# Optimization experiments

Measured on AMD Instinct MI355X. Metric: run time of the kernel, lower is better.

The kernel has to match this reference:

```python
import jax, jax.numpy as jnp
import numpy as np

B, H, S, O = 16384, 512, 6, 1


def setup_inputs() -> dict:
    key = jax.random.key(0)
    ks = jax.random.split(key, 14)
    w = lambda k, shape: jax.random.normal(k, shape, dtype=jnp.float32) * 0.02
    return {
        "input": jax.random.normal(ks[0], (B, O), dtype=jnp.float32),
        "hidden": jax.random.normal(ks[1], (B, H), dtype=jnp.float32),
        "cell": jax.random.normal(ks[2], (B, H), dtype=jnp.float32),
        "encoder_outputs": jax.random.normal(ks[3], (B, S, H), dtype=jnp.float32),
        # attn: Linear(2H+O -> S)
        "W_attn": w(ks[4], (S, 2 * H + O)),
        "b_attn": w(ks[5], (S,)),
        # attn_combine: Linear(H+O -> H)
        "W_comb": w(ks[6], (H, H + O)),
        "b_comb": w(ks[7], (H,)),
        # LSTM(H -> H), torch gate order i,f,g,o
        "W_ih": w(ks[8], (4 * H, H)),
        "W_hh": w(ks[9], (4 * H, H)),
        "b_ih": w(ks[10], (4 * H,)),
        "b_hh": w(ks[11], (4 * H,)),
        # out: Linear(H -> O)
        "W_out": w(ks[12], (O, H)),
        "b_out": w(ks[13], (O,)),
    }


def reference(input, hidden, cell, encoder_outputs,
              W_attn, b_attn, W_comb, b_comb,
              W_ih, W_hh, b_ih, b_hh, W_out, b_out):
    # Bahdanau-style attention over encoder outputs (eval mode: dropout = identity)
    attn_in = jnp.concatenate([input, hidden, cell], axis=1)          # [B, 2H+O]
    attn_weights = jax.nn.softmax(attn_in @ W_attn.T + b_attn, axis=1)  # [B, S]
    attn_applied = jnp.einsum("bs,bsh->bh", attn_weights, encoder_outputs)  # [B, H]

    x = jnp.concatenate([input, attn_applied], axis=1)                # [B, H+O]
    x = jax.nn.relu(x @ W_comb.T + b_comb)                            # [B, H]

    # single LSTM step (torch gate order: i, f, g, o)
    gates = x @ W_ih.T + b_ih + hidden @ W_hh.T + b_hh               # [B, 4H]
    i, f, g, o = jnp.split(gates, 4, axis=1)
    c_new = jax.nn.sigmoid(f) * cell + jax.nn.sigmoid(i) * jnp.tanh(g)
    h_new = jax.nn.sigmoid(o) * jnp.tanh(c_new)

    output = h_new @ W_out.T + b_out                                  # [B, O]
    return output, h_new, c_new, attn_weights[:, None, :]
```

## Files before the change

kernel.cpp:

```cpp
#include <hip/hip_runtime.h>
#include <hip/hip_bf16.h>

typedef __attribute__((ext_vector_type(8))) short frag8;
typedef __attribute__((ext_vector_type(4))) float f32x4;

#define ASYNC16(gsrc, ldst) \
  __builtin_amdgcn_global_load_lds((const __attribute__((address_space(1))) void*)(gsrc), \
                                   (__attribute__((address_space(3))) void*)(ldst), 16, 0, 0)

__device__ __forceinline__ float sigmoid_(float x) { return 1.0f / (1.0f + __expf(-x)); }
__device__ __forceinline__ float tanh_(float x)    { return 1.0f - 2.0f / (__expf(2.0f * x) + 1.0f); }

__global__ __launch_bounds__(256) void prep_kernel(
    const float* __restrict__ W_comb, const float* __restrict__ W_ih,
    const float* __restrict__ W_hh, const float* __restrict__ b_ih,
    const float* __restrict__ b_hh,
    __hip_bfloat16* __restrict__ Wc, __hip_bfloat16* __restrict__ Wg,
    float* __restrict__ biasg)
{
  int idx = blockIdx.x * 256 + threadIdx.x;
  const int NW = 2048 * 1024, NC = 512 * 512;
  if (idx < NW) {
    int np = idx >> 10, k = idx & 1023;
    int u = np >> 2, j = np & 3;
    int n = j * 512 + u;
    float v = (k < 512) ? W_ih[n * 512 + k] : W_hh[n * 512 + (k - 512)];
    Wg[idx] = __float2bfloat16(v);
  } else if (idx < NW + NC) {
    int t = idx - NW;
    int n = t >> 9, k = t & 511;
    Wc[t] = __float2bfloat16(W_comb[n * 513 + 1 + k]);
  } else if (idx < NW + NC + 2048) {
    int np = idx - NW - NC;
    int u = np >> 2, j = np & 3;
    int n = j * 512 + u;
    biasg[np] = b_ih[n] + b_hh[n];
  }
}

__global__ __launch_bounds__(256) void attn_kernel(
    const float* __restrict__ inputv, const float* __restrict__ hidden,
    const float* __restrict__ cell, const float* __restrict__ enc,
    const float* __restrict__ W_attn, const float* __restrict__ b_attn,
    __hip_bfloat16* __restrict__ A1, __hip_bfloat16* __restrict__ Z,
    float* __restrict__ outA)
{
  __shared__ float Wl[6 * 1025];
  const int tid = threadIdx.x;
  for (int i = tid; i < 6 * 1025; i += 256) Wl[i] = W_attn[i];
  __syncthreads();
  const int w = tid >> 6, lane = tid & 63;
  const long row = (long)blockIdx.x * 4 + w;

  const float* hp = hidden + row * 512;
  const float* cp = cell + row * 512;
  float h8[8];
  float acc[6] = {0.f, 0.f, 0.f, 0.f, 0.f, 0.f};
#pragma unroll
  for (int i = 0; i < 8; ++i) {
    int k = lane + i * 64;
    float hv = hp[k], cv = cp[k];
    h8[i] = hv;
#pragma unroll
    for (int s = 0; s < 6; ++s)
      acc[s] += hv * Wl[s * 1025 + 1 + k] + cv * Wl[s * 1025 + 513 + k];
  }
  float iv = inputv[row];
  float logit[6];
#pragma unroll
  for (int s = 0; s < 6; ++s) {
    float a = acc[s];
#pragma unroll
    for (int d = 32; d > 0; d >>= 1) a += __shfl_xor(a, d);
    logit[s] = a + iv * Wl[s * 1025] + b_attn[s];
  }
  float mx = logit[0];
#pragma unroll
  for (int s = 1; s < 6; ++s) mx = fmaxf(mx, logit[s]);
  float wts[6], tot = 0.f;
#pragma unroll
  for (int s = 0; s < 6; ++s) { wts[s] = __expf(logit[s] - mx); tot += wts[s]; }
  float rt = 1.f / tot;
#pragma unroll
  for (int s = 0; s < 6; ++s) wts[s] *= rt;
  if (lane < 6) {
    float mw = 0.f;
#pragma unroll
    for (int s = 0; s < 6; ++s) if (lane == s) mw = wts[s];
    outA[row * 6 + lane] = mw;
  }
  const float* ep = enc + row * 3072;
#pragma unroll
  for (int i = 0; i < 8; ++i) {
    int k = lane + i * 64;
    float a = 0.f;
#pragma unroll
    for (int s = 0; s < 6; ++s) a += wts[s] * ep[s * 512 + k];
    A1[row * 512 + k] = __float2bfloat16(a);
    Z[row * 1024 + 512 + k] = __float2bfloat16(h8[i]);
  }
}

__device__ __forceinline__ void stage16(const __hip_bfloat16* __restrict__ g, int ld,
                                        int row0, int k0, __hip_bfloat16* lds, int tid)
{
  int c0 = tid, c1 = tid + 256;
  const __hip_bfloat16* g0 = g + (long)(row0 + (c0 >> 2)) * ld + k0 + (c0 & 3) * 8;
  const __hip_bfloat16* g1 = g + (long)(row0 + (c1 >> 2)) * ld + k0 + (c1 & 3) * 8;
  char* l0 = (char*)lds + (tid & ~63) * 16;
  ASYNC16(g0, l0);
  ASYNC16(g1, l0 + 4096);
}

__global__ __launch_bounds__(256) void comb_gemm(
    const __hip_bfloat16* __restrict__ A, const __hip_bfloat16* __restrict__ Bt,
    const float* __restrict__ b_comb, const float* __restrict__ W_comb,
    const float* __restrict__ inputv, __hip_bfloat16* __restrict__ Z)
{
  __shared__ __align__(16) __hip_bfloat16 As[128 * 32];
  __shared__ __align__(16) __hip_bfloat16 Bs[128 * 32];
  const int tid = threadIdx.x;
  const int lane = tid & 63, w = tid >> 6;
  const int quad = lane >> 4, l15 = lane & 15;
  const int m0 = blockIdx.y * 128, n0 = blockIdx.x * 128;
  const int wm = (w & 1) * 64, wn = (w >> 1) * 64;

  f32x4 acc[4][4] = {};
  for (int kt = 0; kt < 16; ++kt) {
    int k0 = kt * 32;
    stage16(A, 512, m0, k0, As, tid);
    stage16(Bt, 512, n0, k0, Bs, tid);
    __syncthreads();
    frag8 af[4], bf[4];
#pragma unroll
    for (int i = 0; i < 4; ++i)
      af[i] = *(const frag8*)((const short*)As + (wm + i * 16 + l15) * 32 + quad * 8);
#pragma unroll
    for (int j = 0; j < 4; ++j)
      bf[j] = *(const frag8*)((const short*)Bs + (wn + j * 16 + l15) * 32 + quad * 8);
#pragma unroll
    for (int i = 0; i < 4; ++i)
#pragma unroll
      for (int j = 0; j < 4; ++j)
        acc[i][j] = __builtin_amdgcn_mfma_f32_16x16x32_bf16(af[i], bf[j], acc[i][j], 0, 0, 0);
    __syncthreads();
  }
  float bc[4], w0[4];
#pragma unroll
  for (int j = 0; j < 4; ++j) {
    int col = n0 + wn + j * 16 + l15;
    bc[j] = b_comb[col];
    w0[j] = W_comb[col * 513];
  }
#pragma unroll
  for (int i = 0; i < 4; ++i) {
#pragma unroll
    for (int r = 0; r < 4; ++r) {
      int row = m0 + wm + i * 16 + quad * 4 + r;
      float iv = inputv[row];
#pragma unroll
      for (int j = 0; j < 4; ++j) {
        int col = n0 + wn + j * 16 + l15;
        float v = acc[i][j][r] + bc[j] + iv * w0[j];
        Z[(long)row * 1024 + col] = __float2bfloat16(fmaxf(v, 0.0f));
      }
    }
  }
}

__global__ __launch_bounds__(256) void gates_gemm(
    const __hip_bfloat16* __restrict__ Zm, const __hip_bfloat16* __restrict__ Wg,
    const float* __restrict__ biasg, const float* __restrict__ cell,
    float* __restrict__ outH, float* __restrict__ outC)
{
  __shared__ __align__(16) float smemf[64 * 132];
  __hip_bfloat16* As = (__hip_bfloat16*)smemf;
  __hip_bfloat16* Bs = (__hip_bfloat16*)smemf + 4096;
  float* Cl = smemf;
  const int tid = threadIdx.x;
  const int lane = tid & 63, w = tid >> 6;
  const int quad = lane >> 4, l15 = lane & 15;
  const int m0 = blockIdx.y * 128, n0 = blockIdx.x * 128;
  const int wm = (w & 1) * 64, wn = (w >> 1) * 64;

  f32x4 acc[4][4] = {};
  for (int kt = 0; kt < 32; ++kt) {
    int k0 = kt * 32;
    stage16(Zm, 1024, m0, k0, As, tid);
    stage16(Wg, 1024, n0, k0, Bs, tid);
    __syncthreads();
    frag8 af[4], bf[4];
#pragma unroll
    for (int i = 0; i < 4; ++i)
      af[i] = *(const frag8*)((const short*)As + (wm + i * 16 + l15) * 32 + quad * 8);
#pragma unroll
    for (int j = 0; j < 4; ++j)
      bf[j] = *(const frag8*)((const short*)Bs + (wn + j * 16 + l15) * 32 + quad * 8);
#pragma unroll
    for (int i = 0; i < 4; ++i)
#pragma unroll
      for (int j = 0; j < 4; ++j)
        acc[i][j] = __builtin_amdgcn_mfma_f32_16x16x32_bf16(af[i], bf[j], acc[i][j], 0, 0, 0);
    __syncthreads();
  }
  for (int hh = 0; hh < 2; ++hh) {
    if ((w & 1) == hh) {
#pragma unroll
      for (int i = 0; i < 4; ++i)
#pragma unroll
        for (int j = 0; j < 4; ++j)
#pragma unroll
          for (int r = 0; r < 4; ++r)
            Cl[(i * 16 + quad * 4 + r) * 132 + wn + j * 16 + l15] = acc[i][j][r];
    }
    __syncthreads();
#pragma unroll
    for (int it = 0; it < 8; ++it) {
      int p = tid + it * 256;
      int rl = p >> 5, ul = p & 31;
      long row = m0 + hh * 64 + rl;
      int u = (n0 >> 2) + ul;
      float4 gv = *(const float4*)(Cl + rl * 132 + ul * 4);
      float4 bv = *(const float4*)(biasg + n0 + ul * 4);
      float ig = gv.x + bv.x, fg = gv.y + bv.y, gg = gv.z + bv.z, og = gv.w + bv.w;
      float cv = cell[row * 512 + u];
      float cn = sigmoid_(fg) * cv + sigmoid_(ig) * tanh_(gg);
      float hn = sigmoid_(og) * tanh_(cn);
      outH[row * 512 + u] = hn;
      outC[row * 512 + u] = cn;
    }
    __syncthreads();
  }
}

__global__ __launch_bounds__(256) void out_gemv(
    const float* __restrict__ h, const float* __restrict__ W_out,
    const float* __restrict__ b_out, float* __restrict__ out)
{
  __shared__ float wl[512];
  const int tid = threadIdx.x;
  for (int i = tid; i < 512; i += 256) wl[i] = W_out[i];
  __syncthreads();
  const int w = tid >> 6, lane = tid & 63;
  const long row = (long)blockIdx.x * 4 + w;
  float s = 0.f;
#pragma unroll
  for (int i = 0; i < 8; ++i) {
    int k = lane + i * 64;
    s += h[row * 512 + k] * wl[k];
  }
#pragma unroll
  for (int d = 32; d > 0; d >>= 1) s += __shfl_xor(s, d);
  if (lane == 0) out[row] = s + b_out[0];
}

extern "C" void kernel_launch(void* const* d_in, const int* in_sizes, int n_in,
                              void* d_out, int out_size, void* d_ws, size_t ws_size,
                              hipStream_t stream) {
  const float* inputv = (const float*)d_in[0];
  const float* hidden = (const float*)d_in[1];
  const float* cell   = (const float*)d_in[2];
  const float* enc    = (const float*)d_in[3];
  const float* W_attn = (const float*)d_in[4];
  const float* b_attn = (const float*)d_in[5];
  const float* W_comb = (const float*)d_in[6];
  const float* b_comb = (const float*)d_in[7];
  const float* W_ih   = (const float*)d_in[8];
  const float* W_hh   = (const float*)d_in[9];
  const float* b_ih   = (const float*)d_in[10];
  const float* b_hh   = (const float*)d_in[11];
  const float* W_out  = (const float*)d_in[12];
  const float* b_out  = (const float*)d_in[13];

  float* out  = (float*)d_out;
  float* outO = out;
  float* outH = out + 16384;
  float* outC = out + 8404992;
  float* outA = out + 16793600;

  char* ws = (char*)d_ws;
  __hip_bfloat16* Z   = (__hip_bfloat16*)ws;
  __hip_bfloat16* A1  = (__hip_bfloat16*)(ws + 33554432);
  __hip_bfloat16* Wc  = (__hip_bfloat16*)(ws + 50331648);
  __hip_bfloat16* Wg  = (__hip_bfloat16*)(ws + 50855936);
  float*          bg  = (float*)(ws + 55050240);

  prep_kernel<<<9224, 256, 0, stream>>>(W_comb, W_ih, W_hh, b_ih, b_hh, Wc, Wg, bg);
  attn_kernel<<<4096, 256, 0, stream>>>(inputv, hidden, cell, enc, W_attn, b_attn, A1, Z, outA);
  comb_gemm<<<dim3(4, 128), 256, 0, stream>>>(A1, Wc, b_comb, W_comb, inputv, Z);
  gates_gemm<<<dim3(16, 128), 256, 0, stream>>>(Z, Wg, bg, cell, outH, outC);
  out_gemv<<<4096, 256, 0, stream>>>(outH, W_out, b_out, outO);
}
```

Before: 532.7 us.

## Reorder gate weight interleave for direct epilogue, vectorize loads, widen GEMM K-step

```diff
diff --git a/kernel.cpp b/kernel.cpp
--- a/kernel.cpp
+++ b/kernel.cpp
@@ -22,7 +22,8 @@
   const int NW = 2048 * 1024, NC = 512 * 512;
   if (idx < NW) {
     int np = idx >> 10, k = idx & 1023;
-    int u = np >> 2, j = np & 3;
+    int j = (np >> 4) & 3;
+    int u = ((np >> 6) << 4) | (np & 15);
     int n = j * 512 + u;
     float v = (k < 512) ? W_ih[n * 512 + k] : W_hh[n * 512 + (k - 512)];
     Wg[idx] = __float2bfloat16(v);
@@ -32,7 +33,8 @@
     Wc[t] = __float2bfloat16(W_comb[n * 513 + 1 + k]);
   } else if (idx < NW + NC + 2048) {
     int np = idx - NW - NC;
-    int u = np >> 2, j = np & 3;
+    int j = (np >> 4) & 3;
+    int u = ((np >> 6) << 4) | (np & 15);
     int n = j * 512 + u;
     biasg[np] = b_ih[n] + b_hh[n];
   }
@@ -45,25 +47,34 @@
     __hip_bfloat16* __restrict__ A1, __hip_bfloat16* __restrict__ Z,
     float* __restrict__ outA)
 {
-  __shared__ float Wl[6 * 1025];
+  __shared__ float Wlh[6 * 1024];
+  __shared__ float Wl0[6];
   const int tid = threadIdx.x;
-  for (int i = tid; i < 6 * 1025; i += 256) Wl[i] = W_attn[i];
+  for (int i = tid; i < 6 * 1024; i += 256) {
+    int s = i >> 10, k = i & 1023;
+    Wlh[i] = W_attn[s * 1025 + 1 + k];
+  }
+  if (tid < 6) Wl0[tid] = W_attn[tid * 1025];
   __syncthreads();
   const int w = tid >> 6, lane = tid & 63;
   const long row = (long)blockIdx.x * 4 + w;
-
-  const float* hp = hidden + row * 512;
-  const float* cp = cell + row * 512;
-  float h8[8];
-  float acc[6] = {0.f, 0.f, 0.f, 0.f, 0.f, 0.f};
-#pragma unroll
-  for (int i = 0; i < 8; ++i) {
-    int k = lane + i * 64;
-    float hv = hp[k], cv = cp[k];
-    h8[i] = hv;
-#pragma unroll
-    for (int s = 0; s < 6; ++s)
-      acc[s] += hv * Wl[s * 1025 + 1 + k] + cv * Wl[s * 1025 + 513 + k];
+  const int k8 = lane * 8;
+
+  const float4* hp4 = (const float4*)(hidden + row * 512 + k8);
+  const float4* cp4 = (const float4*)(cell + row * 512 + k8);
+  float4 h0 = hp4[0], h1 = hp4[1];
+  float4 c0 = cp4[0], c1 = cp4[1];
+
+  float acc[6];
+#pragma unroll
+  for (int s = 0; s < 6; ++s) {
+    const float4* wh = (const float4*)(Wlh + s * 1024 + k8);
+    const float4* wc = (const float4*)(Wlh + s * 1024 + 512 + k8);
+    float4 a0 = wh[0], a1 = wh[1], b0 = wc[0], b1 = wc[1];
+    acc[s] = h0.x * a0.x + h0.y * a0.y + h0.z * a0.z + h0.w * a0.w
+           + h1.x * a1.x + h1.y * a1.y + h1.z * a1.z + h1.w * a1.w
+           + c0.x * b0.x + c0.y * b0.y + c0.z * b0.z + c0.w * b0.w
+           + c1.x * b1.x + c1.y * b1.y + c1.z * b1.z + c1.w * b1.w;
   }
   float iv = inputv[row];
   float logit[6];
@@ -72,7 +83,7 @@
     float a = acc[s];
 #pragma unroll
     for (int d = 32; d > 0; d >>= 1) a += __shfl_xor(a, d);
-    logit[s] = a + iv * Wl[s * 1025] + b_attn[s];
+    logit[s] = a + iv * Wl0[s] + b_attn[s];
   }
   float mx = logit[0];
 #pragma unroll
@@ -89,16 +100,22 @@
     for (int s = 0; s < 6; ++s) if (lane == s) mw = wts[s];
     outA[row * 6 + lane] = mw;
   }
-  const float* ep = enc + row * 3072;
-#pragma unroll
-  for (int i = 0; i < 8; ++i) {
-    int k = lane + i * 64;
-    float a = 0.f;
-#pragma unroll
-    for (int s = 0; s < 6; ++s) a += wts[s] * ep[s * 512 + k];
-    A1[row * 512 + k] = __float2bfloat16(a);
-    Z[row * 1024 + 512 + k] = __float2bfloat16(h8[i]);
-  }
+  float a8[8] = {0.f, 0.f, 0.f, 0.f, 0.f, 0.f, 0.f, 0.f};
+  const float* ep = enc + row * 3072 + k8;
+#pragma unroll
+  for (int s = 0; s < 6; ++s) {
+    float4 e0 = *(const float4*)(ep + s * 512);
+    float4 e1 = *(const float4*)(ep + s * 512 + 4);
+    float ws_ = wts[s];
+    a8[0] += ws_ * e0.x; a8[1] += ws_ * e0.y; a8[2] += ws_ * e0.z; a8[3] += ws_ * e0.w;
+    a8[4] += ws_ * e1.x; a8[5] += ws_ * e1.y; a8[6] += ws_ * e1.z; a8[7] += ws_ * e1.w;
+  }
+  union { frag8 v; __hip_bfloat16 h[8]; } pa, ph;
+  float hv8[8] = {h0.x, h0.y, h0.z, h0.w, h1.x, h1.y, h1.z, h1.w};
+#pragma unroll
+  for (int i = 0; i < 8; ++i) { pa.h[i] = __float2bfloat16(a8[i]); ph.h[i] = __float2bfloat16(hv8[i]); }
+  *(frag8*)(A1 + row * 512 + k8) = pa.v;
+  *(frag8*)(Z + row * 1024 + 512 + k8) = ph.v;
 }
 
 __device__ __forceinline__ void stage16(const __hip_bfloat16* __restrict__ g, int ld,
@@ -117,8 +134,8 @@
     const float* __restrict__ b_comb, const float* __restrict__ W_comb,
     const float* __restrict__ inputv, __hip_bfloat16* __restrict__ Z)
 {
-  __shared__ __align__(16) __hip_bfloat16 As[128 * 32];
-  __shared__ __align__(16) __hip_bfloat16 Bs[128 * 32];
+  __shared__ __align__(16) __hip_bfloat16 As[2][128 * 32];
+  __shared__ __align__(16) __hip_bfloat16 Bs[2][128 * 32];
   const int tid = threadIdx.x;
   const int lane = tid & 63, w = tid >> 6;
   const int quad = lane >> 4, l15 = lane & 15;
@@ -126,23 +143,28 @@
   const int wm = (w & 1) * 64, wn = (w >> 1) * 64;
 
   f32x4 acc[4][4] = {};
-  for (int kt = 0; kt < 16; ++kt) {
-    int k0 = kt * 32;
-    stage16(A, 512, m0, k0, As, tid);
-    stage16(Bt, 512, n0, k0, Bs, tid);
+  for (int kt = 0; kt < 8; ++kt) {
+    int k0 = kt * 64;
+    stage16(A, 512, m0, k0, As[0], tid);
+    stage16(A, 512, m0, k0 + 32, As[1], tid);
+    stage16(Bt, 512, n0, k0, Bs[0], tid);
+    stage16(Bt, 512, n0, k0 + 32, Bs[1], tid);
     __syncthreads();
-    frag8 af[4], bf[4];
-#pragma unroll
-    for (int i = 0; i < 4; ++i)
-      af[i] = *(const frag8*)((const short*)As + (wm + i * 16 + l15) * 32 + quad * 8);
-#pragma unroll
-    for (int j = 0; j < 4; ++j)
-      bf[j] = *(const frag8*)((const short*)Bs + (wn + j * 16 + l15) * 32 + quad * 8);
-#pragma unroll
-    for (int i = 0; i < 4; ++i)
+#pragma unroll
+    for (int h = 0; h < 2; ++h) {
+      frag8 af[4], bf[4];
+#pragma unroll
+      for (int i = 0; i < 4; ++i)
+        af[i] = *(const frag8*)((const short*)As[h] + (wm + i * 16 + l15) * 32 + quad * 8);
 #pragma unroll
       for (int j = 0; j < 4; ++j)
-        acc[i][j] = __builtin_amdgcn_mfma_f32_16x16x32_bf16(af[i], bf[j], acc[i][j], 0, 0, 0);
+        bf[j] = *(const frag8*)((const short*)Bs[h] + (wn + j * 16 + l15) * 32 + quad * 8);
+#pragma unroll
+      for (int i = 0; i < 4; ++i)
+#pragma unroll
+        for (int j = 0; j < 4; ++j)
+          acc[i][j] = __builtin_amdgcn_mfma_f32_16x16x32_bf16(af[i], bf[j], acc[i][j], 0, 0, 0);
+    }
     __syncthreads();
   }
   float bc[4], w0[4];
@@ -173,10 +195,8 @@
     const float* __restrict__ biasg, const float* __restrict__ cell,
     float* __restrict__ outH, float* __restrict__ outC)
 {
-  __shared__ __align__(16) float smemf[64 * 132];
-  __hip_bfloat16* As = (__hip_bfloat16*)smemf;
-  __hip_bfloat16* Bs = (__hip_bfloat16*)smemf + 4096;
-  float* Cl = smemf;
+  __shared__ __align__(16) __hip_bfloat16 As[2][128 * 32];
+  __shared__ __align__(16) __hip_bfloat16 Bs[2][128 * 32];
   const int tid = threadIdx.x;
   const int lane = tid & 63, w = tid >> 6;
   const int quad = lane >> 4, l15 = lane & 15;
@@ -184,52 +204,50 @@
   const int wm = (w & 1) * 64, wn = (w >> 1) * 64;
 
   f32x4 acc[4][4] = {};
-  for (int kt = 0; kt < 32; ++kt) {
-    int k0 = kt * 32;
-    stage16(Zm, 1024, m0, k0, As, tid);
-    stage16(Wg, 1024, n0, k0, Bs, tid);
+  for (int kt = 0; kt < 16; ++kt) {
+    int k0 = kt * 64;
+    stage16(Zm, 1024, m0, k0, As[0], tid);
+    stage16(Zm, 1024, m0, k0 + 32, As[1], tid);
+    stage16(Wg, 1024, n0, k0, Bs[0], tid);
+    stage16(Wg, 1024, n0, k0 + 32, Bs[1], tid);
     __syncthreads();
-    frag8 af[4], bf[4];
-#pragma unroll
-    for (int i = 0; i < 4; ++i)
-      af[i] = *(const frag8*)((const short*)As + (wm + i * 16 + l15) * 32 + quad * 8);
-#pragma unroll
-    for (int j = 0; j < 4; ++j)
-      bf[j] = *(const frag8*)((const short*)Bs + (wn + j * 16 + l15) * 32 + quad * 8);
-#pragma unroll
-    for (int i = 0; i < 4; ++i)
+#pragma unroll
+    for (int h = 0; h < 2; ++h) {
+      frag8 af[4], bf[4];
+#pragma unroll
+      for (int i = 0; i < 4; ++i)
+        af[i] = *(const frag8*)((const short*)As[h] + (wm + i * 16 + l15) * 32 + quad * 8);
 #pragma unroll
       for (int j = 0; j < 4; ++j)
-        acc[i][j] = __builtin_amdgcn_mfma_f32_16x16x32_bf16(af[i], bf[j], acc[i][j], 0, 0, 0);
-    __syncthreads();
-  }
-  for (int hh = 0; hh < 2; ++hh) {
-    if ((w & 1) == hh) {
+        bf[j] = *(const frag8*)((const short*)Bs[h] + (wn + j * 16 + l15) * 32 + quad * 8);
 #pragma unroll
       for (int i = 0; i < 4; ++i)
 #pragma unroll
         for (int j = 0; j < 4; ++j)
-#pragma unroll
-          for (int r = 0; r < 4; ++r)
-            Cl[(i * 16 + quad * 4 + r) * 132 + wn + j * 16 + l15] = acc[i][j][r];
+          acc[i][j] = __builtin_amdgcn_mfma_f32_16x16x32_bf16(af[i], bf[j], acc[i][j], 0, 0, 0);
     }
     __syncthreads();
-#pragma unroll
-    for (int it = 0; it < 8; ++it) {
-      int p = tid + it * 256;
-      int rl = p >> 5, ul = p & 31;
-      long row = m0 + hh * 64 + rl;
-      int u = (n0 >> 2) + ul;
-      float4 gv = *(const float4*)(Cl + rl * 132 + ul * 4);
-      float4 bv = *(const float4*)(biasg + n0 + ul * 4);
-      float ig = gv.x + bv.x, fg = gv.y + bv.y, gg = gv.z + bv.z, og = gv.w + bv.w;
+  }
+  const int u = ((n0 + wn) >> 2) + l15;
+  const float bi = biasg[n0 + wn + l15];
+  const float bfg = biasg[n0 + wn + 16 + l15];
+  const float bgg = biasg[n0 + wn + 32 + l15];
+  const float bo = biasg[n0 + wn + 48 + l15];
+#pragma unroll
+  for (int i = 0; i < 4; ++i) {
+#pragma unroll
+    for (int r = 0; r < 4; ++r) {
+      long row = m0 + wm + i * 16 + quad * 4 + r;
       float cv = cell[row * 512 + u];
+      float ig = acc[i][0][r] + bi;
+      float fg = acc[i][1][r] + bfg;
+      float gg = acc[i][2][r] + bgg;
+      float og = acc[i][3][r] + bo;
       float cn = sigmoid_(fg) * cv + sigmoid_(ig) * tanh_(gg);
       float hn = sigmoid_(og) * tanh_(cn);
       outH[row * 512 + u] = hn;
       outC[row * 512 + u] = cn;
     }
-    __syncthreads();
   }
 }
 
@@ -243,12 +261,13 @@
   __syncthreads();
   const int w = tid >> 6, lane = tid & 63;
   const long row = (long)blockIdx.x * 4 + w;
-  float s = 0.f;
-#pragma unroll
-  for (int i = 0; i < 8; ++i) {
-    int k = lane + i * 64;
-    s += h[row * 512 + k] * wl[k];
-  }
+  const int k8 = lane * 8;
+  const float4* hp4 = (const float4*)(h + row * 512 + k8);
+  const float4* wp4 = (const float4*)(wl + k8);
+  float4 h0 = hp4[0], h1 = hp4[1];
+  float4 w0 = wp4[0], w1 = wp4[1];
+  float s = h0.x * w0.x + h0.y * w0.y + h0.z * w0.z + h0.w * w0.w
+          + h1.x * w1.x + h1.y * w1.y + h1.z * w1.z + h1.w * w1.w;
 #pragma unroll
   for (int d = 32; d > 0; d >>= 1) s += __shfl_xor(s, d);
   if (lane == 0) out[row] = s + b_out[0];
```

After: 503.9 us. 5.4% less time.
